# Performance work log

Hardware: AMD Instinct MI355X
Metric: run time of the kernel (lower is better)

## Reference

```python
import jax, jax.numpy as jnp
import numpy as np

N_NODES = 50000
N_EDGES = 800000
IN_DIM = 128
OUT_DIM = 64


def setup_inputs() -> dict:
    key = jax.random.key(0)
    k1, k2, k3, k4, k5 = jax.random.split(key, 5)
    x = jax.random.normal(k1, (N_NODES, IN_DIM), dtype=jnp.float32)
    edge_src = jax.random.randint(k2, (N_EDGES,), 0, N_NODES, dtype=jnp.int64)
    edge_dst = jax.random.randint(k3, (N_EDGES,), 0, N_NODES, dtype=jnp.int64)
    edge_weight = jax.random.uniform(k4, (N_EDGES,), dtype=jnp.float32)
    # Glorot-uniform weight as in weight_variable_glorot (range = sqrt(6/input_dim))
    init_range = np.sqrt(6.0 / IN_DIM).astype(np.float32)
    w = jax.random.uniform(k5, (IN_DIM, OUT_DIM), minval=-init_range,
                           maxval=init_range, dtype=jnp.float32)
    return {"x": x, "edge_src": edge_src, "edge_dst": edge_dst,
            "edge_weight": edge_weight, "w": w}


def reference(x, edge_src, edge_dst, edge_weight, w):
    # Dense projection: [N, in] @ [in, out] -> [N, out]
    h = x @ w
    # Sparse adjacency matmul (adj @ h) in COO form:
    # out[dst] += weight * h[src]
    msgs = edge_weight[:, None] * h[edge_src]          # [E, out]
    agg = jax.ops.segment_sum(msgs, edge_dst, num_segments=N_NODES)
    return jax.nn.relu(agg)
```

## Files before the change

### kernel.cpp

```cpp
#include <hip/hip_runtime.h>

#define N_NODES 50000
#define N_EDGES 800000
#define IN_DIM 128
#define OUT_DIM 64
#define ROWS 64

__global__ __launch_bounds__(256, 2) void gc_gemm(const float* __restrict__ x,
                                                  const float* __restrict__ w,
                                                  float* __restrict__ h) {
    __shared__ float w_lds[IN_DIM * OUT_DIM];
    __shared__ float x_lds[ROWS * IN_DIM];

    const int tid = threadIdx.x;
    const int row0 = blockIdx.x * ROWS;

    const float4* w4 = reinterpret_cast<const float4*>(w);
    float4* wl4 = reinterpret_cast<float4*>(w_lds);
#pragma unroll
    for (int i = 0; i < 8; ++i) wl4[tid + i * 256] = w4[tid + i * 256];

    const float4* x4 = reinterpret_cast<const float4*>(x);
    float4* xl4 = reinterpret_cast<float4*>(x_lds);
#pragma unroll
    for (int i = 0; i < 8; ++i) {
        const int idx = tid + i * 256;
        const int r = idx >> 5;
        const int kc = idx & 31;
        const int g = row0 + r;
        float4 v = make_float4(0.f, 0.f, 0.f, 0.f);
        if (g < N_NODES) v = x4[(size_t)g * 32 + kc];
        xl4[r * 32 + (kc ^ (r & 3))] = v;
    }
    __syncthreads();

    const int tx = tid & 15;
    const int ty = tid >> 4;
    const int sw = ty & 3;

    float4 acc[4];
#pragma unroll
    for (int i = 0; i < 4; ++i) acc[i] = make_float4(0.f, 0.f, 0.f, 0.f);

    for (int kc = 0; kc < 32; ++kc) {
        float4 xv[4], wv[4];
#pragma unroll
        for (int i = 0; i < 4; ++i)
            xv[i] = xl4[(ty + 16 * i) * 32 + (kc ^ sw)];
#pragma unroll
        for (int j = 0; j < 4; ++j)
            wv[j] = wl4[(kc * 4 + j) * 16 + tx];
#pragma unroll
        for (int i = 0; i < 4; ++i) {
            acc[i].x = fmaf(xv[i].x, wv[0].x, acc[i].x);
            acc[i].y = fmaf(xv[i].x, wv[0].y, acc[i].y);
            acc[i].z = fmaf(xv[i].x, wv[0].z, acc[i].z);
            acc[i].w = fmaf(xv[i].x, wv[0].w, acc[i].w);
            acc[i].x = fmaf(xv[i].y, wv[1].x, acc[i].x);
            acc[i].y = fmaf(xv[i].y, wv[1].y, acc[i].y);
            acc[i].z = fmaf(xv[i].y, wv[1].z, acc[i].z);
            acc[i].w = fmaf(xv[i].y, wv[1].w, acc[i].w);
            acc[i].x = fmaf(xv[i].z, wv[2].x, acc[i].x);
            acc[i].y = fmaf(xv[i].z, wv[2].y, acc[i].y);
            acc[i].z = fmaf(xv[i].z, wv[2].z, acc[i].z);
            acc[i].w = fmaf(xv[i].z, wv[2].w, acc[i].w);
            acc[i].x = fmaf(xv[i].w, wv[3].x, acc[i].x);
            acc[i].y = fmaf(xv[i].w, wv[3].y, acc[i].y);
            acc[i].z = fmaf(xv[i].w, wv[3].z, acc[i].z);
            acc[i].w = fmaf(xv[i].w, wv[3].w, acc[i].w);
        }
    }

    float4* h4 = reinterpret_cast<float4*>(h);
#pragma unroll
    for (int i = 0; i < 4; ++i) {
        const int r = row0 + ty + 16 * i;
        if (r < N_NODES) h4[(size_t)r * 16 + tx] = acc[i];
    }
}

__global__ __launch_bounds__(256) void gc_scatter(const float* __restrict__ h,
                                                  const int* __restrict__ esrc,
                                                  const int* __restrict__ edst,
                                                  const float* __restrict__ ew,
                                                  float* __restrict__ out) {
    const int e = __builtin_amdgcn_readfirstlane(blockIdx.x * 4 + (threadIdx.x >> 6));
    const int d = threadIdx.x & 63;

    const int s = esrc[e];
    const int t = edst[e];
    const float v = ew[e] * h[(size_t)s * OUT_DIM + d];
    atomicAdd(&out[(size_t)t * OUT_DIM + d], v);
}

__global__ __launch_bounds__(256) void gc_relu(float* __restrict__ out) {
    const int i = blockIdx.x * 256 + threadIdx.x;
    const int n4 = N_NODES * OUT_DIM / 4;
    if (i < n4) {
        float4* o4 = reinterpret_cast<float4*>(out);
        float4 v = o4[i];
        v.x = fmaxf(v.x, 0.0f);
        v.y = fmaxf(v.y, 0.0f);
        v.z = fmaxf(v.z, 0.0f);
        v.w = fmaxf(v.w, 0.0f);
        o4[i] = v;
    }
}

extern "C" void kernel_launch(void* const* d_in, const int* in_sizes, int n_in,
                              void* d_out, int out_size, void* d_ws, size_t ws_size,
                              hipStream_t stream) {
    const float* x    = (const float*)d_in[0];
    const int*   esrc = (const int*)d_in[1];
    const int*   edst = (const int*)d_in[2];
    const float* ew   = (const float*)d_in[3];
    const float* w    = (const float*)d_in[4];
    float* out = (float*)d_out;
    float* h   = (float*)d_ws;

    hipMemsetAsync(d_out, 0, (size_t)N_NODES * OUT_DIM * sizeof(float), stream);

    gc_gemm<<<(N_NODES + ROWS - 1) / ROWS, 256, 0, stream>>>(x, w, h);

    gc_scatter<<<N_EDGES / 4, 256, 0, stream>>>(h, esrc, edst, ew, out);

    gc_relu<<<(N_NODES * OUT_DIM / 4 + 255) / 256, 256, 0, stream>>>(out);
}
```

Before: 273.5 us.

## Replace atomic COO scatter with per-call CSR build and pull-based aggregation

Each call now builds a destination-sorted CSR: it histograms the destinations, runs a single-block exclusive scan, and reorders sources and weights with atomic slot claims. A gather kernel then assigns one wavefront per destination node, accumulates in registers and applies the ReLU inline. This removes 51.2M float atomics, the output memset and the separate ReLU pass. In exchange it adds several small launches, a serial single-block scan and 1.6M integer atomics. The edge order within each row is nondeterministic, so the float summation order varies between runs.

```diff
diff --git a/kernel.cpp b/kernel.cpp
--- a/kernel.cpp
+++ b/kernel.cpp
@@ -79,32 +79,89 @@
     }
 }
 
-__global__ __launch_bounds__(256) void gc_scatter(const float* __restrict__ h,
-                                                  const int* __restrict__ esrc,
+__global__ __launch_bounds__(256) void gc_hist(const int* __restrict__ edst,
+                                               int* __restrict__ offs) {
+    const int e = blockIdx.x * 256 + threadIdx.x;
+    atomicAdd(&offs[edst[e]], 1);
+}
+
+#define SCAN_CHUNK 196
+__global__ __launch_bounds__(256) void gc_scan(int* __restrict__ offs) {
+    __shared__ int part[256];
+    const int t = threadIdx.x;
+    const int base = t * SCAN_CHUNK;
+    const int n = (base < N_NODES) ? min(SCAN_CHUNK, N_NODES - base) : 0;
+
+    int sum = 0;
+    for (int i = 0; i < n; ++i) sum += offs[base + i];
+    part[t] = sum;
+    __syncthreads();
+
+    for (int off = 1; off < 256; off <<= 1) {
+        int v = (t >= off) ? part[t - off] : 0;
+        __syncthreads();
+        part[t] += v;
+        __syncthreads();
+    }
+
+    int run = part[t] - sum;
+    for (int i = 0; i < n; ++i) {
+        int c = offs[base + i];
+        offs[base + i] = run;
+        run += c;
+    }
+}
+
+__global__ __launch_bounds__(256) void gc_reorder(const int* __restrict__ esrc,
                                                   const int* __restrict__ edst,
                                                   const float* __restrict__ ew,
-                                                  float* __restrict__ out) {
-    const int e = __builtin_amdgcn_readfirstlane(blockIdx.x * 4 + (threadIdx.x >> 6));
-    const int d = threadIdx.x & 63;
-
-    const int s = esrc[e];
-    const int t = edst[e];
-    const float v = ew[e] * h[(size_t)s * OUT_DIM + d];
-    atomicAdd(&out[(size_t)t * OUT_DIM + d], v);
+                                                  int* __restrict__ offs,
+                                                  int* __restrict__ csr_src,
+                                                  float* __restrict__ csr_w) {
+    const int e = blockIdx.x * 256 + threadIdx.x;
+    const int d = edst[e];
+    const int pos = atomicAdd(&offs[d], 1);
+    csr_src[pos] = esrc[e];
+    csr_w[pos] = ew[e];
 }
 
-__global__ __launch_bounds__(256) void gc_relu(float* __restrict__ out) {
-    const int i = blockIdx.x * 256 + threadIdx.x;
-    const int n4 = N_NODES * OUT_DIM / 4;
-    if (i < n4) {
-        float4* o4 = reinterpret_cast<float4*>(out);
-        float4 v = o4[i];
-        v.x = fmaxf(v.x, 0.0f);
-        v.y = fmaxf(v.y, 0.0f);
-        v.z = fmaxf(v.z, 0.0f);
-        v.w = fmaxf(v.w, 0.0f);
-        o4[i] = v;
+__global__ __launch_bounds__(256) void gc_aggregate(const float* __restrict__ h,
+                                                    const int* __restrict__ offs,
+                                                    const int* __restrict__ csr_src,
+                                                    const float* __restrict__ csr_w,
+                                                    float* __restrict__ out) {
+    const int node = __builtin_amdgcn_readfirstlane(blockIdx.x * 4 + (threadIdx.x >> 6));
+    const int lane = threadIdx.x & 63;
+
+    const int beg = __builtin_amdgcn_readfirstlane(node ? offs[node - 1] : 0);
+    const int end = __builtin_amdgcn_readfirstlane(offs[node]);
+
+    float acc = 0.0f;
+    int j = beg;
+    for (; j + 4 <= end; j += 4) {
+        const int s0 = __builtin_amdgcn_readfirstlane(csr_src[j + 0]);
+        const int s1 = __builtin_amdgcn_readfirstlane(csr_src[j + 1]);
+        const int s2 = __builtin_amdgcn_readfirstlane(csr_src[j + 2]);
+        const int s3 = __builtin_amdgcn_readfirstlane(csr_src[j + 3]);
+        const float w0 = csr_w[j + 0];
+        const float w1 = csr_w[j + 1];
+        const float w2 = csr_w[j + 2];
+        const float w3 = csr_w[j + 3];
+        const float v0 = h[(size_t)s0 * OUT_DIM + lane];
+        const float v1 = h[(size_t)s1 * OUT_DIM + lane];
+        const float v2 = h[(size_t)s2 * OUT_DIM + lane];
+        const float v3 = h[(size_t)s3 * OUT_DIM + lane];
+        acc = fmaf(w0, v0, acc);
+        acc = fmaf(w1, v1, acc);
+        acc = fmaf(w2, v2, acc);
+        acc = fmaf(w3, v3, acc);
     }
+    for (; j < end; ++j) {
+        const int s = __builtin_amdgcn_readfirstlane(csr_src[j]);
+        acc = fmaf(csr_w[j], h[(size_t)s * OUT_DIM + lane], acc);
+    }
+
+    out[(size_t)node * OUT_DIM + lane] = fmaxf(acc, 0.0f);
 }
 
 extern "C" void kernel_launch(void* const* d_in, const int* in_sizes, int n_in,
@@ -116,13 +173,18 @@
     const float* ew   = (const float*)d_in[3];
     const float* w    = (const float*)d_in[4];
     float* out = (float*)d_out;
-    float* h   = (float*)d_ws;
 
-    hipMemsetAsync(d_out, 0, (size_t)N_NODES * OUT_DIM * sizeof(float), stream);
+    float* h       = (float*)d_ws;
+    int*   offs    = (int*)(h + (size_t)N_NODES * OUT_DIM);
+    int*   csr_src = offs + 50048;
+    float* csr_w   = (float*)(csr_src + N_EDGES);
 
     gc_gemm<<<(N_NODES + ROWS - 1) / ROWS, 256, 0, stream>>>(x, w, h);
 
-    gc_scatter<<<N_EDGES / 4, 256, 0, stream>>>(h, esrc, edst, ew, out);
+    hipMemsetAsync(offs, 0, (size_t)N_NODES * sizeof(int), stream);
+    gc_hist<<<N_EDGES / 256, 256, 0, stream>>>(edst, offs);
+    gc_scan<<<1, 256, 0, stream>>>(offs);
+    gc_reorder<<<N_EDGES / 256, 256, 0, stream>>>(esrc, edst, ew, offs, csr_src, csr_w);
 
-    gc_relu<<<(N_NODES * OUT_DIM / 4 + 255) / 256, 256, 0, stream>>>(out);
+    gc_aggregate<<<N_NODES / 4, 256, 0, stream>>>(h, offs, csr_src, csr_w, out);
 }
```

Result: slower. 297.9 us (+8.9%).

## Bin edges by destination block and aggregate in LDS with bf16 features

Applied to the files above, without the earlier changes.

Replaces the global atomic scatter with a counting-sort pass that groups edges into 64-node destination bins (histogram, scan, per-chunk staged binning). A per-bin kernel then accumulates in an LDS tile with shared-memory atomics and applies ReLU on writeback, which removes the output memset and the separate ReLU pass. The projected features are stored as bf16 to halve gather traffic. The cost is extra preprocessing launches and reduced precision in h, and src/dst are packed into 16 bits each, which truncates node ids above 65535.

```diff
diff --git a/kernel.cpp b/kernel.cpp
--- a/kernel.cpp
+++ b/kernel.cpp
@@ -5,10 +5,23 @@
 #define IN_DIM 128
 #define OUT_DIM 64
 #define ROWS 64
+#define NB 782
+#define BIN_CHUNK 4096
+#define NBIN ((N_EDGES + BIN_CHUNK - 1) / BIN_CHUNK)
+
+__device__ __forceinline__ unsigned short f2bf(float f) {
+    unsigned u = __builtin_bit_cast(unsigned, f);
+    u += 0x7FFF + ((u >> 16) & 1);
+    return (unsigned short)(u >> 16);
+}
+__device__ __forceinline__ float bf2f(unsigned short u) {
+    unsigned x = ((unsigned)u) << 16;
+    return __builtin_bit_cast(float, x);
+}
 
 __global__ __launch_bounds__(256, 2) void gc_gemm(const float* __restrict__ x,
                                                   const float* __restrict__ w,
-                                                  float* __restrict__ h) {
+                                                  unsigned short* __restrict__ h16) {
     __shared__ float w_lds[IN_DIM * OUT_DIM];
     __shared__ float x_lds[ROWS * IN_DIM];
 
@@ -71,39 +84,204 @@
         }
     }
 
-    float4* h4 = reinterpret_cast<float4*>(h);
+    ushort4* h4 = reinterpret_cast<ushort4*>(h16);
 #pragma unroll
     for (int i = 0; i < 4; ++i) {
         const int r = row0 + ty + 16 * i;
-        if (r < N_NODES) h4[(size_t)r * 16 + tx] = acc[i];
-    }
-}
-
-__global__ __launch_bounds__(256) void gc_scatter(const float* __restrict__ h,
-                                                  const int* __restrict__ esrc,
-                                                  const int* __restrict__ edst,
-                                                  const float* __restrict__ ew,
-                                                  float* __restrict__ out) {
-    const int e = __builtin_amdgcn_readfirstlane(blockIdx.x * 4 + (threadIdx.x >> 6));
-    const int d = threadIdx.x & 63;
-
-    const int s = esrc[e];
-    const int t = edst[e];
-    const float v = ew[e] * h[(size_t)s * OUT_DIM + d];
-    atomicAdd(&out[(size_t)t * OUT_DIM + d], v);
-}
-
-__global__ __launch_bounds__(256) void gc_relu(float* __restrict__ out) {
-    const int i = blockIdx.x * 256 + threadIdx.x;
-    const int n4 = N_NODES * OUT_DIM / 4;
-    if (i < n4) {
-        float4* o4 = reinterpret_cast<float4*>(out);
-        float4 v = o4[i];
-        v.x = fmaxf(v.x, 0.0f);
-        v.y = fmaxf(v.y, 0.0f);
-        v.z = fmaxf(v.z, 0.0f);
-        v.w = fmaxf(v.w, 0.0f);
-        o4[i] = v;
+        if (r < N_NODES) {
+            ushort4 o;
+            o.x = f2bf(acc[i].x);
+            o.y = f2bf(acc[i].y);
+            o.z = f2bf(acc[i].z);
+            o.w = f2bf(acc[i].w);
+            h4[(size_t)r * 16 + tx] = o;
+        }
+    }
+}
+
+__global__ __launch_bounds__(512) void gc_bhist(const int* __restrict__ edst,
+                                                int* __restrict__ bcnt) {
+    __shared__ int lh[NB];
+    const int t = threadIdx.x;
+    for (int i = t; i < NB; i += 512) lh[i] = 0;
+    __syncthreads();
+    const int base = blockIdx.x * BIN_CHUNK;
+#pragma unroll
+    for (int k = 0; k < 8; ++k) {
+        const int e = base + k * 512 + t;
+        if (e < N_EDGES) atomicAdd(&lh[edst[e] >> 6], 1);
+    }
+    __syncthreads();
+    for (int i = t; i < NB; i += 512) {
+        const int c = lh[i];
+        if (c) atomicAdd(&bcnt[i], c);
+    }
+}
+
+__global__ __launch_bounds__(1024) void gc_bscan(const int* __restrict__ bcnt,
+                                                 int* __restrict__ bstart,
+                                                 int* __restrict__ bcur) {
+    __shared__ int part[1024];
+    const int t = threadIdx.x;
+    const int v = (t < NB) ? bcnt[t] : 0;
+    part[t] = v;
+    __syncthreads();
+#pragma unroll
+    for (int off = 1; off < 1024; off <<= 1) {
+        const int u = (t >= off) ? part[t - off] : 0;
+        __syncthreads();
+        part[t] += u;
+        __syncthreads();
+    }
+    if (t < NB) {
+        const int ex = part[t] - v;
+        bstart[t] = ex;
+        bcur[t] = ex;
+    }
+}
+
+__global__ __launch_bounds__(512) void gc_bin(const int* __restrict__ esrc,
+                                              const int* __restrict__ edst,
+                                              const float* __restrict__ ew,
+                                              int* __restrict__ bcur,
+                                              int2* __restrict__ tmp) {
+    __shared__ int2 stage[BIN_CHUNK];
+    __shared__ int lh[NB];
+    __shared__ int lbase[NB];
+    __shared__ int lcur[NB];
+    __shared__ int part[512];
+
+    const int t = threadIdx.x;
+    const int base = blockIdx.x * BIN_CHUNK;
+
+    for (int i = t; i < NB; i += 512) lh[i] = 0;
+    __syncthreads();
+
+    int2 rec[8];
+    int bkt[8];
+    bool val[8];
+#pragma unroll
+    for (int k = 0; k < 8; ++k) {
+        const int e = base + k * 512 + t;
+        val[k] = (e < N_EDGES);
+        if (val[k]) {
+            const int d = edst[e];
+            rec[k] = make_int2((int)(((unsigned)d << 16) | (unsigned)esrc[e]),
+                               __float_as_int(ew[e]));
+            bkt[k] = d >> 6;
+            atomicAdd(&lh[bkt[k]], 1);
+        }
+    }
+    __syncthreads();
+
+    {
+        int s = 0;
+        if (t < 391) s = lh[2 * t] + lh[2 * t + 1];
+        part[t] = s;
+        __syncthreads();
+#pragma unroll
+        for (int off = 1; off < 512; off <<= 1) {
+            const int u = (t >= off) ? part[t - off] : 0;
+            __syncthreads();
+            part[t] += u;
+            __syncthreads();
+        }
+        if (t < 391) {
+            const int pre = part[t] - s;
+            lbase[2 * t] = pre;
+            lcur[2 * t] = pre;
+            lbase[2 * t + 1] = pre + lh[2 * t];
+            lcur[2 * t + 1] = pre + lh[2 * t];
+        }
+    }
+    __syncthreads();
+
+#pragma unroll
+    for (int k = 0; k < 8; ++k)
+        if (val[k]) {
+            const int p = atomicAdd(&lcur[bkt[k]], 1);
+            stage[p] = rec[k];
+        }
+    __syncthreads();
+
+    const int wv = t >> 6, ln = t & 63;
+    for (int b = wv; b < NB; b += 8) {
+        const int cnt = lh[b];
+        if (!cnt) continue;
+        int gbase;
+        if (ln == 0) gbase = atomicAdd(&bcur[b], cnt);
+        gbase = __builtin_amdgcn_readfirstlane(gbase);
+        const int lb = lbase[b];
+        for (int i = ln; i < cnt; i += 64) tmp[gbase + i] = stage[lb + i];
+    }
+}
+
+__global__ __launch_bounds__(256) void gc_bagg(const unsigned short* __restrict__ h16,
+                                               const int* __restrict__ bstart,
+                                               const int* __restrict__ bcur,
+                                               const int2* __restrict__ tmp,
+                                               float* __restrict__ out) {
+    __shared__ float tile[64 * 64];
+    const int t = threadIdx.x;
+    const int b = blockIdx.x;
+
+    float4* t4 = reinterpret_cast<float4*>(tile);
+    for (int i = t; i < 1024; i += 256) t4[i] = make_float4(0.f, 0.f, 0.f, 0.f);
+    __syncthreads();
+
+    const int beg = bstart[b];
+    const int end = bcur[b];
+    const int wv = t >> 6, ln = t & 63;
+
+    const int cnt = end - beg;
+    const int wbeg = beg + (int)(((long long)cnt * wv) >> 2);
+    const int wend = beg + (int)(((long long)cnt * (wv + 1)) >> 2);
+
+    int j = wbeg;
+    for (; j + 8 <= wend; j += 8) {
+        unsigned pk[8];
+        float wt[8];
+#pragma unroll
+        for (int k = 0; k < 8; ++k) {
+            const int2 r = tmp[j + k];
+            pk[k] = (unsigned)__builtin_amdgcn_readfirstlane(r.x);
+            wt[k] = __int_as_float(__builtin_amdgcn_readfirstlane(r.y));
+        }
+        float v[8];
+#pragma unroll
+        for (int k = 0; k < 8; ++k) {
+            const int src = (int)(pk[k] & 0xFFFFu);
+            v[k] = bf2f(h16[(size_t)src * OUT_DIM + ln]);
+        }
+#pragma unroll
+        for (int k = 0; k < 8; ++k) {
+            const int row = (int)((pk[k] >> 16) & 63u);
+            atomicAdd(&tile[row * 64 + ln], wt[k] * v[k]);
+        }
+    }
+    for (; j < wend; ++j) {
+        const int2 r = tmp[j];
+        const unsigned p = (unsigned)__builtin_amdgcn_readfirstlane(r.x);
+        const float wt = __int_as_float(__builtin_amdgcn_readfirstlane(r.y));
+        const int src = (int)(p & 0xFFFFu);
+        const int row = (int)((p >> 16) & 63u);
+        atomicAdd(&tile[row * 64 + ln], wt * bf2f(h16[(size_t)src * OUT_DIM + ln]));
+    }
+    __syncthreads();
+
+    float4* o4 = reinterpret_cast<float4*>(out);
+    const int node0 = b * 64;
+    for (int i = t; i < 1024; i += 256) {
+        const int r = i >> 4;
+        const int g = node0 + r;
+        if (g < N_NODES) {
+            float4 vv = t4[i];
+            vv.x = fmaxf(vv.x, 0.f);
+            vv.y = fmaxf(vv.y, 0.f);
+            vv.z = fmaxf(vv.z, 0.f);
+            vv.w = fmaxf(vv.w, 0.f);
+            o4[(size_t)g * 16 + (i & 15)] = vv;
+        }
     }
 }
 
@@ -116,13 +294,19 @@
     const float* ew   = (const float*)d_in[3];
     const float* w    = (const float*)d_in[4];
     float* out = (float*)d_out;
-    float* h   = (float*)d_ws;
-
-    hipMemsetAsync(d_out, 0, (size_t)N_NODES * OUT_DIM * sizeof(float), stream);
-
-    gc_gemm<<<(N_NODES + ROWS - 1) / ROWS, 256, 0, stream>>>(x, w, h);
-
-    gc_scatter<<<N_EDGES / 4, 256, 0, stream>>>(h, esrc, edst, ew, out);
-
-    gc_relu<<<(N_NODES * OUT_DIM / 4 + 255) / 256, 256, 0, stream>>>(out);
-}
+
+    unsigned short* h16 = (unsigned short*)d_ws;
+    int*  bcnt   = (int*)(h16 + (size_t)N_NODES * OUT_DIM);
+    int*  bstart = bcnt + 800;
+    int*  bcur   = bstart + 800;
+    int2* tmp    = (int2*)(bcur + 800 + 16);
+
+    gc_gemm<<<(N_NODES + ROWS - 1) / ROWS, 256, 0, stream>>>(x, w, h16);
+
+    hipMemsetAsync(bcnt, 0, NB * sizeof(int), stream);
+    gc_bhist<<<NBIN, 512, 0, stream>>>(edst, bcnt);
+    gc_bscan<<<1, 1024, 0, stream>>>(bcnt, bstart, bcur);
+    gc_bin<<<NBIN, 512, 0, stream>>>(esrc, edst, ew, bcur, tmp);
+
+    gc_bagg<<<NB, 256, 0, stream>>>(h16, bstart, bcur, tmp, out);
+}
```

Result: slower. 693.3 us (+153.4%).
